# Kernel tuning notes

Hardware: AMD Instinct MI355X
Metric: run time of the kernel (lower is better)

## Reference

```python
import jax, jax.numpy as jnp
import numpy as np

N = 100000      # nodes
E = 640000      # edges
V_IN = 128
U_IN = 64
HID = 128
B = 128         # graphs


def setup_inputs() -> dict:
    key = jax.random.key(0)
    ks = jax.random.split(key, 9)
    x = jax.random.normal(ks[0], (N, V_IN), dtype=jnp.float32)
    edge_index = jax.random.randint(ks[1], (2, E), 0, N, dtype=jnp.int64)
    edge_attr = jax.random.normal(ks[2], (E, HID), dtype=jnp.float32)
    u = jax.random.normal(ks[3], (B, U_IN), dtype=jnp.float32)
    batch = jnp.sort(jax.random.randint(ks[4], (N,), 0, B, dtype=jnp.int64))
    fan_in1 = V_IN + HID + U_IN
    W1 = jax.random.normal(ks[5], (fan_in1, HID), dtype=jnp.float32) / np.sqrt(fan_in1)
    b1 = jnp.zeros((HID,), dtype=jnp.float32)
    W2 = jax.random.normal(ks[6], (HID, HID), dtype=jnp.float32) / np.sqrt(HID)
    b2 = jnp.zeros((HID,), dtype=jnp.float32)
    return {"x": x, "edge_index": edge_index, "edge_attr": edge_attr, "u": u,
            "batch": batch, "W1": W1, "b1": b1, "W2": W2, "b2": b2}


def reference(x, edge_index, edge_attr, u, batch, W1, b1, W2, b2):
    col = edge_index[1]
    # scatter_add edge_attr into destination-node slots: [N, HID]
    agg = jax.ops.segment_sum(edge_attr, col, num_segments=x.shape[0])
    # concat [x, agg, u[batch]] -> [N, V_IN + HID + U_IN]
    h = jnp.concatenate([x, agg, u[batch]], axis=1)
    h = jax.nn.relu(h @ W1 + b1)
    return h @ W2 + b2
```

## Files before the change

kernel.cpp:

```cpp
#include <hip/hip_runtime.h>
#include <hip/hip_bf16.h>

#define V_IN 128
#define U_IN 64
#define HID 128
#define K1  (V_IN + HID + U_IN)

typedef __attribute__((ext_vector_type(8))) short bf16x8;
typedef __attribute__((ext_vector_type(4))) float f32x4;

static __device__ __forceinline__ unsigned short f2bf(float f) {
    __hip_bfloat16 h = __float2bfloat16(f);
    union { __hip_bfloat16 h; unsigned short u; } v; v.h = h;
    return v.u;
}
static __device__ __forceinline__ unsigned int f2bf2(float lo, float hi) {
    __hip_bfloat162 h2 = __float22bfloat162_rn(make_float2(lo, hi));
    union { __hip_bfloat162 h; unsigned int u; } v; v.h = h2;
    return v.u;
}

__global__ __launch_bounds__(256) void zero_prep(
    const float* __restrict__ W1, const float* __restrict__ W2,
    unsigned short* __restrict__ Wt1, unsigned short* __restrict__ Wt2,
    int* __restrict__ deg, int N)
{
    int id = blockIdx.x * 256 + threadIdx.x;
    if (id < N) deg[id] = 0;
    if (id < HID * K1) {
        int c = id / K1, k = id - c * K1;
        Wt1[id] = f2bf(W1[(size_t)k * HID + c]);
    }
    if (id < HID * HID) {
        int c = id >> 7, k = id & 127;
        Wt2[id] = f2bf(W2[(size_t)k * HID + c]);
    }
}


__global__ __launch_bounds__(256) void hist_kernel(
    const int* __restrict__ col, int* __restrict__ deg, int E)
{
    int e = blockIdx.x * 256 + threadIdx.x;
    if (e < E) atomicAdd(&deg[col[e]], 1);
}

__global__ __launch_bounds__(256) void scan_partial(
    const int* __restrict__ deg, int* __restrict__ blockSums, int N)
{
    __shared__ int sdata[256];
    int base = blockIdx.x * 1024;
    int tid  = threadIdx.x;
    int s = 0;
    #pragma unroll
    for (int j = 0; j < 4; ++j) {
        int i = base + tid * 4 + j;
        if (i < N) s += deg[i];
    }
    sdata[tid] = s;
    __syncthreads();
    for (int off = 128; off > 0; off >>= 1) {
        if (tid < off) sdata[tid] += sdata[tid + off];
        __syncthreads();
    }
    if (tid == 0) blockSums[blockIdx.x] = sdata[0];
}

__global__ __launch_bounds__(256) void scan_final(
    const int* __restrict__ deg, const int* __restrict__ blockSums,
    int* __restrict__ offsets, int* __restrict__ cur, int N, int E)
{
    __shared__ int sdata[256];
    __shared__ int rdata[256];
    int tid = threadIdx.x;

    int part = 0;
    for (int i = tid; i < (int)blockIdx.x; i += 256) part += blockSums[i];
    rdata[tid] = part;
    __syncthreads();
    for (int off = 128; off > 0; off >>= 1) {
        if (tid < off) rdata[tid] += rdata[tid + off];
        __syncthreads();
    }
    const int blockPrefix = rdata[0];

    int base = blockIdx.x * 1024;
    int loc[4];
    int s = 0;
    #pragma unroll
    for (int j = 0; j < 4; ++j) {
        int i = base + tid * 4 + j;
        loc[j] = (i < N) ? deg[i] : 0;
        s += loc[j];
    }
    int mine = s;
    sdata[tid] = s;
    __syncthreads();
    for (int off = 1; off < 256; off <<= 1) {
        int t = (tid >= off) ? sdata[tid - off] : 0;
        __syncthreads();
        sdata[tid] += t;
        __syncthreads();
    }
    int prefix = blockPrefix + sdata[tid] - mine;
    #pragma unroll
    for (int j = 0; j < 4; ++j) {
        int i = base + tid * 4 + j;
        if (i < N) { offsets[i] = prefix; cur[i] = prefix; prefix += loc[j]; }
    }
    if (blockIdx.x == 0 && tid == 0) offsets[N] = E;
}

__global__ __launch_bounds__(256) void fill_kernel(
    const int* __restrict__ col, int* __restrict__ cur,
    int* __restrict__ eidx, int E)
{
    int e = blockIdx.x * 256 + threadIdx.x;
    if (e < E) {
        int p = atomicAdd(&cur[col[e]], 1);
        eidx[p] = e;
    }
}

#define ROWS 32
#define LDA_E 328
#define LDH_E 136
#define ECAP 1280

__global__ __launch_bounds__(512, 4) void mlp_mfma(
    const float* __restrict__ x,
    const float* __restrict__ edge_attr,
    const int*   __restrict__ offsets,
    const int*   __restrict__ eidx,
    const float* __restrict__ u,
    const int*   __restrict__ batch,
    const unsigned short* __restrict__ Wt1,
    const unsigned short* __restrict__ Wt2,
    const float* __restrict__ b1, const float* __restrict__ b2,
    float* __restrict__ out, int N)
{
    __shared__ __align__(16) unsigned short A[ROWS * LDA_E];
    __shared__ __align__(16) unsigned short H[ROWS * LDH_E];
    __shared__ int Eidx[ECAP];
    __shared__ int Soff[ROWS + 1];
    const int tid  = threadIdx.x;
    const int n0   = blockIdx.x * ROWS;
    const int lane = tid & 63;
    const int wave = tid >> 6;
    const int l15  = lane & 15;
    const int lhi  = lane >> 4;
    const int wcol = wave * 16 + l15;

    const int nEnd   = (n0 + ROWS < N) ? n0 + ROWS : N;
    if (tid <= ROWS) {
        int idx = n0 + tid;
        Soff[tid] = offsets[(idx < nEnd) ? idx : nEnd];
    }
    const int s_base = offsets[n0];
    const int s_end  = offsets[nEnd];
    const int cnt    = (s_end - s_base < ECAP) ? s_end - s_base : ECAP;
    for (int i = tid; i < cnt; i += 512) Eidx[i] = eidx[s_base + i];

    #pragma unroll
    for (int it = 0; it < 3; ++it) {
        int t   = tid + it * 512;
        int row = t / 48;
        int s   = t - row * 48;
        int n   = n0 + row;
        unsigned short* Arow = &A[row * LDA_E];
        float4 v = make_float4(0.f, 0.f, 0.f, 0.f);
        int colbase;
        if (s < 32) {
            if (n < N) v = ((const float4*)(x + (size_t)n * V_IN))[s];
            colbase = s * 4;
        } else {
            if (n < N) {
                int b = batch[n];
                v = ((const float4*)(u + (size_t)b * U_IN))[s - 32];
            }
            colbase = V_IN + HID + (s - 32) * 4;
        }
        uint2 o; o.x = f2bf2(v.x, v.y); o.y = f2bf2(v.z, v.w);
        *(uint2*)&Arow[colbase] = o;
    }
    __syncthreads();

    #pragma unroll
    for (int it = 0; it < 2; ++it) {
        int t   = tid + it * 512;
        int row = t >> 5;
        int c   = t & 31;
        int n   = n0 + row;
        f32x4 a0 = {0.f, 0.f, 0.f, 0.f};
        f32x4 a1 = {0.f, 0.f, 0.f, 0.f};
        f32x4 a2 = {0.f, 0.f, 0.f, 0.f};
        f32x4 a3 = {0.f, 0.f, 0.f, 0.f};
        if (n < N) {
            int ls = Soff[row]     - s_base;
            int le = Soff[row + 1] - s_base;
            int j = ls;
            for (; j + 3 < le; j += 4) {
                int e0, e1, e2, e3;
                if (j + 3 < ECAP) {
                    e0 = Eidx[j];     e1 = Eidx[j + 1];
                    e2 = Eidx[j + 2]; e3 = Eidx[j + 3];
                } else {
                    e0 = eidx[s_base + j];     e1 = eidx[s_base + j + 1];
                    e2 = eidx[s_base + j + 2]; e3 = eidx[s_base + j + 3];
                }
                f32x4 v0 = __builtin_nontemporal_load((const f32x4*)(edge_attr + (size_t)e0 * HID) + c);
                f32x4 v1 = __builtin_nontemporal_load((const f32x4*)(edge_attr + (size_t)e1 * HID) + c);
                f32x4 v2 = __builtin_nontemporal_load((const f32x4*)(edge_attr + (size_t)e2 * HID) + c);
                f32x4 v3 = __builtin_nontemporal_load((const f32x4*)(edge_attr + (size_t)e3 * HID) + c);
                a0 += v0; a1 += v1; a2 += v2; a3 += v3;
            }
            for (; j < le; ++j) {
                int e0 = (j < ECAP) ? Eidx[j] : eidx[s_base + j];
                a0 += __builtin_nontemporal_load((const f32x4*)(edge_attr + (size_t)e0 * HID) + c);
            }
        }
        f32x4 asum = (a0 + a1) + (a2 + a3);
        uint2 o;
        o.x = f2bf2(asum[0], asum[1]);
        o.y = f2bf2(asum[2], asum[3]);
        *(uint2*)&A[row * LDA_E + V_IN + c * 4] = o;
    }

    bf16x8 w1f[10], w2f[4];
    #pragma unroll
    for (int ks = 0; ks < 10; ++ks)
        w1f[ks] = *(const bf16x8*)(Wt1 + (size_t)wcol * K1 + ks * 32 + lhi * 8);
    #pragma unroll
    for (int ks = 0; ks < 4; ++ks)
        w2f[ks] = *(const bf16x8*)(Wt2 + (size_t)wcol * HID + ks * 32 + lhi * 8);
    const float b1v = b1[wcol];
    const float b2v = b2[wcol];

    __syncthreads();

    f32x4 acc[2] = {{0.f, 0.f, 0.f, 0.f}, {0.f, 0.f, 0.f, 0.f}};
    #pragma unroll
    for (int ks = 0; ks < 10; ++ks) {
        #pragma unroll
        for (int h = 0; h < 2; ++h) {
            bf16x8 af = *(const bf16x8*)&A[(h * 16 + l15) * LDA_E + ks * 32 + lhi * 8];
            acc[h] = __builtin_amdgcn_mfma_f32_16x16x32_bf16(af, w1f[ks], acc[h], 0, 0, 0);
        }
    }
    #pragma unroll
    for (int h = 0; h < 2; ++h)
        #pragma unroll
        for (int r = 0; r < 4; ++r) {
            float hv = fmaxf(acc[h][r] + b1v, 0.f);
            H[(h * 16 + lhi * 4 + r) * LDH_E + wcol] = f2bf(hv);
        }
    __syncthreads();

    f32x4 acc2[2] = {{0.f, 0.f, 0.f, 0.f}, {0.f, 0.f, 0.f, 0.f}};
    #pragma unroll
    for (int ks = 0; ks < 4; ++ks) {
        #pragma unroll
        for (int h = 0; h < 2; ++h) {
            bf16x8 hf = *(const bf16x8*)&H[(h * 16 + l15) * LDH_E + ks * 32 + lhi * 8];
            acc2[h] = __builtin_amdgcn_mfma_f32_16x16x32_bf16(hf, w2f[ks], acc2[h], 0, 0, 0);
        }
    }
    #pragma unroll
    for (int h = 0; h < 2; ++h)
        #pragma unroll
        for (int r = 0; r < 4; ++r) {
            int n = n0 + h * 16 + lhi * 4 + r;
            if (n < N) out[(size_t)n * HID + wcol] = acc2[h][r] + b2v;
        }
}

extern "C" void kernel_launch(void* const* d_in, const int* in_sizes, int n_in,
                              void* d_out, int out_size, void* d_ws, size_t ws_size,
                              hipStream_t stream) {
    const float* x          = (const float*)d_in[0];
    const int*   edge_index = (const int*)  d_in[1];
    const float* edge_attr  = (const float*)d_in[2];
    const float* u          = (const float*)d_in[3];
    const int*   batch      = (const int*)  d_in[4];
    const float* W1         = (const float*)d_in[5];
    const float* b1         = (const float*)d_in[6];
    const float* W2         = (const float*)d_in[7];
    const float* b2         = (const float*)d_in[8];
    float* out = (float*)d_out;

    const int N = in_sizes[0] / V_IN;
    const int E = in_sizes[1] / 2;
    const int* col = edge_index + E;

    unsigned short* Wt1  = (unsigned short*)d_ws;
    unsigned short* Wt2  = Wt1 + (size_t)K1 * HID;
    int* deg       = (int*)(Wt2 + (size_t)HID * HID);
    int* cur       = deg + N;
    int* offsets   = cur + N;
    int* blockSums = offsets + N + 1;
    int* eidx      = blockSums + 2048;

    const int NB = (N + 1023) / 1024;
    const int ZP = ((N > HID * K1 ? N : HID * K1) + 255) / 256;

    zero_prep   <<<ZP, 256, 0, stream>>>(W1, W2, Wt1, Wt2, deg, N);
    hist_kernel <<<(E + 255) / 256, 256, 0, stream>>>(col, deg, E);
    scan_partial<<<NB, 256, 0, stream>>>(deg, blockSums, N);
    scan_final  <<<NB, 256, 0, stream>>>(deg, blockSums, offsets, cur, N, E);
    fill_kernel <<<(E + 255) / 256, 256, 0, stream>>>(col, cur, eidx, E);

    mlp_mfma<<<(N + ROWS - 1) / ROWS, 512, 0, stream>>>(
        x, edge_attr, offsets, eidx, u, batch, Wt1, Wt2, b1, b2, out, N);
}
```

Baseline: 201.5 us.

## Parallelize edge aggregation over edges with LDS float atomics instead of per-row loops

```diff
diff --git a/kernel.cpp b/kernel.cpp
--- a/kernel.cpp
+++ b/kernel.cpp
@@ -141,8 +141,9 @@
 {
     __shared__ __align__(16) unsigned short A[ROWS * LDA_E];
     __shared__ __align__(16) unsigned short H[ROWS * LDH_E];
-    __shared__ int Eidx[ECAP];
-    __shared__ int Soff[ROWS + 1];
+    __shared__ float Af[ROWS * HID];
+    __shared__ int  Eidx[ECAP];
+    __shared__ int  Soff[ROWS + 1];
     const int tid  = threadIdx.x;
     const int n0   = blockIdx.x * ROWS;
     const int lane = tid & 63;
@@ -151,15 +152,14 @@
     const int lhi  = lane >> 4;
     const int wcol = wave * 16 + l15;
 
-    const int nEnd   = (n0 + ROWS < N) ? n0 + ROWS : N;
+    const int nEnd = (n0 + ROWS < N) ? n0 + ROWS : N;
     if (tid <= ROWS) {
         int idx = n0 + tid;
         Soff[tid] = offsets[(idx < nEnd) ? idx : nEnd];
     }
-    const int s_base = offsets[n0];
-    const int s_end  = offsets[nEnd];
-    const int cnt    = (s_end - s_base < ECAP) ? s_end - s_base : ECAP;
-    for (int i = tid; i < cnt; i += 512) Eidx[i] = eidx[s_base + i];
+    #pragma unroll
+    for (int it = 0; it < (ROWS * HID) / 512; ++it)
+        Af[tid + it * 512] = 0.f;
 
     #pragma unroll
     for (int it = 0; it < 3; ++it) {
@@ -185,45 +185,80 @@
     }
     __syncthreads();
 
-    #pragma unroll
-    for (int it = 0; it < 2; ++it) {
-        int t   = tid + it * 512;
-        int row = t >> 5;
-        int c   = t & 31;
-        int n   = n0 + row;
-        f32x4 a0 = {0.f, 0.f, 0.f, 0.f};
-        f32x4 a1 = {0.f, 0.f, 0.f, 0.f};
-        f32x4 a2 = {0.f, 0.f, 0.f, 0.f};
-        f32x4 a3 = {0.f, 0.f, 0.f, 0.f};
-        if (n < N) {
-            int ls = Soff[row]     - s_base;
-            int le = Soff[row + 1] - s_base;
-            int j = ls;
-            for (; j + 3 < le; j += 4) {
-                int e0, e1, e2, e3;
-                if (j + 3 < ECAP) {
-                    e0 = Eidx[j];     e1 = Eidx[j + 1];
-                    e2 = Eidx[j + 2]; e3 = Eidx[j + 3];
-                } else {
-                    e0 = eidx[s_base + j];     e1 = eidx[s_base + j + 1];
-                    e2 = eidx[s_base + j + 2]; e3 = eidx[s_base + j + 3];
+    const int s_base = Soff[0];
+    const int total  = Soff[ROWS] - s_base;
+    const int cnt    = (total < ECAP) ? total : ECAP;
+    for (int i = tid; i < cnt; i += 512) {
+        int j = s_base + i;
+        int e = eidx[j];
+        int lo = 0, hi = ROWS;
+        #pragma unroll
+        for (int st = 0; st < 5; ++st) {
+            int mid = (lo + hi) >> 1;
+            if (Soff[mid] <= j) lo = mid; else hi = mid;
+        }
+        Eidx[i] = (e << 5) | lo;
+    }
+    __syncthreads();
+
+    {
+        const int T = cnt * 32;
+        int idx = tid;
+        for (; idx + 512 < T; idx += 1024) {
+            int jA = idx >> 5,        cA = idx & 31;
+            int jB = (idx + 512) >> 5, cB = (idx + 512) & 31;
+            int pkA = Eidx[jA], pkB = Eidx[jB];
+            const float* rpA = edge_attr + ((size_t)(pkA >> 5)) * HID;
+            const float* rpB = edge_attr + ((size_t)(pkB >> 5)) * HID;
+            int rbA = (pkA & 31) * HID, rbB = (pkB & 31) * HID;
+            float vA0 = __builtin_nontemporal_load(rpA + 0  * 32 + cA);
+            float vA1 = __builtin_nontemporal_load(rpA + 1  * 32 + cA);
+            float vA2 = __builtin_nontemporal_load(rpA + 2  * 32 + cA);
+            float vA3 = __builtin_nontemporal_load(rpA + 3  * 32 + cA);
+            float vB0 = __builtin_nontemporal_load(rpB + 0  * 32 + cB);
+            float vB1 = __builtin_nontemporal_load(rpB + 1  * 32 + cB);
+            float vB2 = __builtin_nontemporal_load(rpB + 2  * 32 + cB);
+            float vB3 = __builtin_nontemporal_load(rpB + 3  * 32 + cB);
+            atomicAdd(&Af[rbA + 0 * 32 + cA], vA0);
+            atomicAdd(&Af[rbA + 1 * 32 + cA], vA1);
+            atomicAdd(&Af[rbA + 2 * 32 + cA], vA2);
+            atomicAdd(&Af[rbA + 3 * 32 + cA], vA3);
+            atomicAdd(&Af[rbB + 0 * 32 + cB], vB0);
+            atomicAdd(&Af[rbB + 1 * 32 + cB], vB1);
+            atomicAdd(&Af[rbB + 2 * 32 + cB], vB2);
+            atomicAdd(&Af[rbB + 3 * 32 + cB], vB3);
+        }
+        for (; idx < T; idx += 512) {
+            int j = idx >> 5, c = idx & 31;
+            int pk = Eidx[j];
+            const float* rp = edge_attr + ((size_t)(pk >> 5)) * HID;
+            int rb = (pk & 31) * HID;
+            #pragma unroll
+            for (int w = 0; w < 4; ++w) {
+                float v = __builtin_nontemporal_load(rp + w * 32 + c);
+                atomicAdd(&Af[rb + w * 32 + c], v);
+            }
+        }
+        if (total > cnt) {
+            const int T2 = (total - cnt) * 32;
+            for (int idx2 = tid; idx2 < T2; idx2 += 512) {
+                int j = idx2 >> 5, c = idx2 & 31;
+                int gj = s_base + ECAP + j;
+                int e  = eidx[gj];
+                int lo = 0, hi = ROWS;
+                #pragma unroll
+                for (int st = 0; st < 5; ++st) {
+                    int mid = (lo + hi) >> 1;
+                    if (Soff[mid] <= gj) lo = mid; else hi = mid;
                 }
-                f32x4 v0 = __builtin_nontemporal_load((const f32x4*)(edge_attr + (size_t)e0 * HID) + c);
-                f32x4 v1 = __builtin_nontemporal_load((const f32x4*)(edge_attr + (size_t)e1 * HID) + c);
-                f32x4 v2 = __builtin_nontemporal_load((const f32x4*)(edge_attr + (size_t)e2 * HID) + c);
-                f32x4 v3 = __builtin_nontemporal_load((const f32x4*)(edge_attr + (size_t)e3 * HID) + c);
-                a0 += v0; a1 += v1; a2 += v2; a3 += v3;
+                const float* rp = edge_attr + (size_t)e * HID;
+                #pragma unroll
+                for (int w = 0; w < 4; ++w) {
+                    float v = __builtin_nontemporal_load(rp + w * 32 + c);
+                    atomicAdd(&Af[lo * HID + w * 32 + c], v);
+                }
             }
-            for (; j < le; ++j) {
-                int e0 = (j < ECAP) ? Eidx[j] : eidx[s_base + j];
-                a0 += __builtin_nontemporal_load((const f32x4*)(edge_attr + (size_t)e0 * HID) + c);
-            }
-        }
-        f32x4 asum = (a0 + a1) + (a2 + a3);
-        uint2 o;
-        o.x = f2bf2(asum[0], asum[1]);
-        o.y = f2bf2(asum[2], asum[3]);
-        *(uint2*)&A[row * LDA_E + V_IN + c * 4] = o;
+        }
     }
 
     bf16x8 w1f[10], w2f[4];
@@ -236,6 +271,17 @@
     const float b1v = b1[wcol];
     const float b2v = b2[wcol];
 
+    __syncthreads();
+
+    #pragma unroll
+    for (int it = 0; it < (ROWS * HID / 2) / 512; ++it) {
+        int i   = tid + it * 512;
+        int row = i >> 6;
+        int p   = i & 63;
+        float lo = Af[row * HID + p * 2];
+        float hi = Af[row * HID + p * 2 + 1];
+        *(unsigned int*)&A[row * LDA_E + V_IN + p * 2] = f2bf2(lo, hi);
+    }
     __syncthreads();
 
     f32x4 acc[2] = {{0.f, 0.f, 0.f, 0.f}, {0.f, 0.f, 0.f, 0.f}};
```

Result: slower. 547.1 us (+171.6%).
